# Optimization experiments

Measured on AMD Instinct MI355X. Metric: run time of the kernel, lower is better.

## Reference

```python
import jax, jax.numpy as jnp
import numpy as np

B, F, V, K, D, H = 16384, 26, 100000, 16, 13, 400
IN_DIM = F * K + D  # 429
EPS = 1e-5


def _bn(x, g, b):
    # BatchNorm1d in training mode: batch statistics (biased var, like torch)
    m = jnp.mean(x, axis=0)
    v = jnp.mean((x - m) ** 2, axis=0)
    return g * (x - m) / jnp.sqrt(v + EPS) + b


def setup_inputs() -> dict:
    key = jax.random.key(0)
    ks = jax.random.split(key, 12)
    X_cat = jax.random.randint(ks[0], (B, F), 0, V)
    X_dense = jax.random.normal(ks[1], (B, D), dtype=jnp.float32)
    fm1_tables = jax.random.normal(ks[2], (F, V, 1), dtype=jnp.float32) * 0.01
    emb_tables = jax.random.normal(ks[3], (F, V, K), dtype=jnp.float32) * 0.01
    Wd = jax.random.normal(ks[4], (D, 1), dtype=jnp.float32) * 0.1
    bd = jnp.zeros((1,), jnp.float32)
    W1 = jax.random.normal(ks[5], (IN_DIM, H), dtype=jnp.float32) * (1.0 / np.sqrt(IN_DIM))
    b1 = jnp.zeros((H,), jnp.float32)
    g1 = jnp.ones((H,), jnp.float32)
    be1 = jnp.zeros((H,), jnp.float32)
    W2 = jax.random.normal(ks[6], (H, H), dtype=jnp.float32) * (1.0 / np.sqrt(H))
    b2 = jnp.zeros((H,), jnp.float32)
    g2 = jnp.ones((H,), jnp.float32)
    be2 = jnp.zeros((H,), jnp.float32)
    W3 = jax.random.normal(ks[7], (H, 1), dtype=jnp.float32) * (1.0 / np.sqrt(H))
    b3 = jnp.zeros((1,), jnp.float32)
    return dict(X_cat=X_cat, X_dense=X_dense, fm1_tables=fm1_tables,
                emb_tables=emb_tables, Wd=Wd, bd=bd, W1=W1, b1=b1, g1=g1,
                be1=be1, W2=W2, b2=b2, g2=g2, be2=be2, W3=W3, b3=b3)


def reference(X_cat, X_dense, fm1_tables, emb_tables, Wd, bd,
              W1, b1, g1, be1, W2, b2, g2, be2, W3, b3):
    gather = jax.vmap(lambda tab, idx: tab[idx], in_axes=(0, 1), out_axes=1)
    # 1st order: [B, F, 1] -> sum over fields -> [B, 1]
    y_1st = jnp.sum(gather(fm1_tables, X_cat), axis=1) + X_dense @ Wd + bd
    # 2nd order embeddings: [B, F, K]
    emb = gather(emb_tables, X_cat)
    s = jnp.sum(emb, axis=1)                 # [B, K]
    ix = s ** 2 - jnp.sum(emb ** 2, axis=1)  # [B, K]
    fm_y = 0.5 * jnp.sum(ix, axis=1, keepdims=True)
    # DNN on [flattened embeddings, dense]
    x = jnp.concatenate([emb.reshape(emb.shape[0], -1), X_dense], axis=1)
    h = jax.nn.relu(_bn(x @ W1 + b1, g1, be1))
    h = jax.nn.relu(_bn(h @ W2 + b2, g2, be2))
    dnn_y = h @ W3 + b3
    return y_1st + fm_y + dnn_y
```

## Files before the change

kernel.cpp:

```cpp
#include <hip/hip_runtime.h>
#include <stdint.h>

#define B_ROWS 16384
#define NF 26
#define NV 100000
#define ND 13
#define NH 400
#define XPAD 448
#define ZPAD 416
#define EPS 1e-5f

typedef __attribute__((ext_vector_type(8))) short short8;
typedef __attribute__((ext_vector_type(4))) float f32x4;
typedef __attribute__((ext_vector_type(4))) unsigned int uint4v;

__device__ inline float bf2f(unsigned short u) {
    union { unsigned int i; float f; } v; v.i = (unsigned int)u << 16; return v.f;
}
__device__ inline unsigned short f2bf(float f) {
    union { float f; unsigned int i; } v; v.f = f;
    return (unsigned short)((v.i + 0x7fff + ((v.i >> 16) & 1)) >> 16);
}

typedef __attribute__((address_space(1))) const unsigned int g_u32;
typedef __attribute__((address_space(3))) unsigned int l_u32;
__device__ __forceinline__ void gload_lds16(const void* g, void* l) {
    __builtin_amdgcn_global_load_lds((g_u32*)g, (l_u32*)l, 16, 0, 0);
}

#define X_OFF    0
#define Z1_OFF   14680064
#define W1S_OFF  28311552
#define W2S_OFF  28712960
#define BASE_OFF 29085696
#define ST_OFF   29151232

__global__ __launch_bounds__(256) void gather_prep(
    const int* __restrict__ Xcat, const float* __restrict__ Xdense,
    const float* __restrict__ fm1, const float* __restrict__ emb,
    const float* __restrict__ Wd, const float* __restrict__ bd,
    const float* __restrict__ W1, const float* __restrict__ W2,
    unsigned short* __restrict__ X, float* __restrict__ base,
    unsigned short* __restrict__ W1s, unsigned short* __restrict__ W2s,
    float* __restrict__ st)
{
    int tid = threadIdx.x;
    if (blockIdx.x >= 1024) {
        int c = (blockIdx.x - 1024) * 256 + tid;
        if (c < 256) {
            for (int i = tid; i < 6656; i += 256) st[i] = 0.f;
        }
        const float* W; unsigned short* dst; int K; int cc;
        if (c < 25088) { W = W1; dst = W1s; K = 429; cc = c; }
        else           { W = W2; dst = W2s; K = 400; cc = c - 25088; }
        int n  = cc % 448;
        int q  = (cc / 448) & 3;
        int kt = cc / 1792;
        unsigned short o[8];
        #pragma unroll
        for (int j = 0; j < 8; ++j) {
            int k = kt * 32 + q * 8 + j;
            float v = (n < NH && k < K) ? W[(size_t)k * NH + n] : 0.f;
            o[j] = f2bf(v);
        }
        *(uint4v*)(dst + (size_t)cc * 8) = *(uint4v*)o;
        return;
    }
    int r = blockIdx.x * 16 + (tid >> 4);
    int k = tid & 15;
    const int* idxp = Xcat + (size_t)r * NF;
    unsigned short* xrow = X + (size_t)r * XPAD;

    float s = 0.f, ss = 0.f;
    #pragma unroll
    for (int f = 0; f < NF; ++f) {
        int idx = idxp[f];
        float v = emb[((size_t)f * NV + idx) * 16 + k];
        s += v; ss += v * v;
        xrow[f * 16 + k] = f2bf(v);
    }
    float fmsum = fm1[(size_t)k * NV + idxp[k]];
    if (k < NF - 16) fmsum += fm1[(size_t)(k + 16) * NV + idxp[k + 16]];
    float dsum = 0.f;
    if (k < ND) {
        float xd = Xdense[(size_t)r * ND + k];
        dsum = xd * Wd[k];
        xrow[NF * 16 + k] = f2bf(xd);
    }
    xrow[429 + k] = 0;
    if (k < 3) xrow[445 + k] = 0;

    float ix = s * s - ss;
    float rf = fmsum, rd = dsum;
    #pragma unroll
    for (int off = 8; off; off >>= 1) {
        ix += __shfl_xor(ix, off, 16);
        rf += __shfl_xor(rf, off, 16);
        rd += __shfl_xor(rd, off, 16);
    }
    if (k == 0) base[r] = 0.5f * ix + rf + rd + bd[0];
}

template<int NT, int LDA, bool APPLY_BN>
__global__ __launch_bounds__(512, 2) void gemm_v5(
    const unsigned short* __restrict__ A,
    const unsigned short* __restrict__ Wst,
    const float* __restrict__ bias,
    const float* __restrict__ st_all,
    const float* __restrict__ g, const float* __restrict__ be,
    unsigned short* __restrict__ Z, int ldz, int padZ,
    float* __restrict__ st_out, int sumOff, int sqOff)
{
    __shared__ __align__(16) unsigned short slices[51200];
    __shared__ float alpha_s[416], beta_s[416];

    const int tid = threadIdx.x, bid = blockIdx.x;
    const int lane = tid & 63, wv = tid >> 6;
    const int rg = wv >> 2, w4 = wv & 3;
    const int l15 = lane & 15, qh = lane >> 4;
    const int cb = (w4 == 0) ? 0 : (112 + (w4 - 1) * 96);
    const int NFW = (w4 == 0) ? 7 : 6;
    const int soff = rg * 12800 + ((w4 == 0) ? 0 : (3584 + (w4 - 1) * 3072));
    const int arowA = bid * 64 + rg * 32 + l15;
    const int arowB = arowA + 16;

    if constexpr (APPLY_BN) {
        if (tid < 416) {
            int c = tid;
            float a = 0.f, b = 0.f;
            if (c < NH) {
                float gs = 0.f, gq = 0.f;
                #pragma unroll
                for (int cp = 0; cp < 4; ++cp) {
                    gs += st_all[cp * 1664 + c];
                    gq += st_all[cp * 1664 + 416 + c];
                }
                float mean = gs * (1.f / 16384.f);
                float var  = gq * (1.f / 16384.f) - mean * mean;
                a = g[c] * rsqrtf(var + EPS);
                b = be[c] - mean * a;
            }
            alpha_s[c] = a; beta_s[c] = b;
        }
        __syncthreads();
    }

    f32x4 acc0[7], acc1[7];
    #pragma unroll
    for (int i = 0; i < 7; ++i) { acc0[i] = f32x4{0,0,0,0}; acc1[i] = f32x4{0,0,0,0}; }

    auto stageW = [&](int kt, int buf) {
        unsigned short* sl = slices + buf * 25600 + soff;
        #pragma unroll
        for (int i = 0; i < 7; ++i) if (i < NFW) {
            int ci = (kt * 4 + qh) * 448 + cb + i * 16 + l15;
            gload_lds16(Wst + (size_t)ci * 8, sl + i * 512);
        }
    };
    auto ldA = [&](int kt, short8& a, short8& b) {
        a = *(const short8*)(A + (size_t)arowA * LDA + kt * 32 + qh * 8);
        b = *(const short8*)(A + (size_t)arowB * LDA + kt * 32 + qh * 8);
    };
    auto waitN = [&]() {
        if (w4 == 0) asm volatile("s_waitcnt vmcnt(9)" ::: "memory");
        else         asm volatile("s_waitcnt vmcnt(8)" ::: "memory");
        __builtin_amdgcn_sched_barrier(0);
    };
    auto wait0 = [&]() {
        asm volatile("s_waitcnt vmcnt(0)" ::: "memory");
        __builtin_amdgcn_sched_barrier(0);
    };
    auto waitlg = [&]() {
        asm volatile("s_waitcnt lgkmcnt(0)" ::: "memory");
        __builtin_amdgcn_sched_barrier(0);
    };

    auto phase = [&](int kt, int buf, bool last, bool issue,
                     short8& afA, short8& afB) {
        if (last) wait0(); else waitN();
        const unsigned short* sl = slices + buf * 25600 + soff;
        short8 bf[7];
        #pragma unroll
        for (int i = 0; i < 7; ++i) if (i < NFW)
            bf[i] = *(const short8*)(sl + i * 512 + lane * 8);
        short8 aA = afA, aB = afB;
        waitlg();
        if (issue) { stageW(kt + 2, buf); ldA(kt + 2, afA, afB); }
        if constexpr (APPLY_BN) {
            const int k0 = kt * 32 + qh * 8;
            #pragma unroll
            for (int j = 0; j < 8; ++j) {
                float al = alpha_s[k0 + j], bt = beta_s[k0 + j];
                aA[j] = (short)f2bf(fmaxf(0.f, al * bf2f((unsigned short)aA[j]) + bt));
                aB[j] = (short)f2bf(fmaxf(0.f, al * bf2f((unsigned short)aB[j]) + bt));
            }
        }
        #pragma unroll
        for (int i = 0; i < 7; ++i) if (i < NFW) {
            acc0[i] = __builtin_amdgcn_mfma_f32_16x16x32_bf16(aA, bf[i], acc0[i], 0, 0, 0);
            acc1[i] = __builtin_amdgcn_mfma_f32_16x16x32_bf16(aB, bf[i], acc1[i], 0, 0, 0);
        }
    };

    short8 afA0, afB0, afA1, afB1;
    stageW(0, 0); ldA(0, afA0, afB0);
    stageW(1, 1); ldA(1, afA1, afB1);

    int kt2 = 0;
    for (; kt2 + 3 < NT; kt2 += 2) {
        phase(kt2,     0, false, true, afA0, afB0);
        phase(kt2 + 1, 1, false, true, afA1, afB1);
    }
    if constexpr (NT % 2 == 0) {
        phase(NT - 2, 0, false, false, afA0, afB0);
        phase(NT - 1, 1, true,  false, afA1, afB1);
    } else {
        phase(NT - 3, 0, false, true,  afA0, afB0);
        phase(NT - 2, 1, false, false, afA1, afB1);
        phase(NT - 1, 0, true,  false, afA0, afB0);
    }

    float* stc = st_out + (bid & 3) * 1664;
    #pragma unroll
    for (int i = 0; i < 7; ++i) if (i < NFW) {
        int col = cb + i * 16 + l15;
        float bv = bias[col];
        float ps = 0.f, pq = 0.f;
        #pragma unroll
        for (int q = 0; q < 4; ++q) {
            float v0 = acc0[i][q] + bv;
            float v1 = acc1[i][q] + bv;
            Z[(size_t)(bid * 64 + rg * 32 + qh * 4 + q) * ldz + col] = f2bf(v0);
            Z[(size_t)(bid * 64 + rg * 32 + 16 + qh * 4 + q) * ldz + col] = f2bf(v1);
            ps += v0 + v1; pq += v0 * v0 + v1 * v1;
        }
        ps += __shfl_xor(ps, 16, 64); ps += __shfl_xor(ps, 32, 64);
        pq += __shfl_xor(pq, 16, 64); pq += __shfl_xor(pq, 32, 64);
        if (qh == 0) {
            atomicAdd(&stc[sumOff + col], ps);
            atomicAdd(&stc[sqOff + col], pq);
        }
    }
    if (padZ && w4 == 3) {
        #pragma unroll
        for (int rr = 0; rr < 8; ++rr)
            Z[(size_t)(bid * 64 + rg * 32 + rr * 4 + qh) * ldz + 400 + l15] = 0;
    }
}

__global__ __launch_bounds__(256) void final_kernel(
    const unsigned short* __restrict__ Z2,
    const float* __restrict__ st_all,
    const float* __restrict__ g2, const float* __restrict__ be2,
    const float* __restrict__ W3, const float* __restrict__ b3,
    const float* __restrict__ base, float* __restrict__ out)
{
    __shared__ float a2s[NH], b2s[NH], w3s[NH];
    int tid = threadIdx.x;
    for (int c = tid; c < NH; c += 256) {
        float gs = 0.f, gq = 0.f;
        #pragma unroll
        for (int cp = 0; cp < 4; ++cp) {
            gs += st_all[cp * 1664 + 832 + c];
            gq += st_all[cp * 1664 + 1248 + c];
        }
        float mean = gs * (1.f / 16384.f);
        float var  = gq * (1.f / 16384.f) - mean * mean;
        float a = g2[c] * rsqrtf(var + EPS);
        a2s[c] = a;
        b2s[c] = be2[c] - mean * a;
        w3s[c] = W3[c];
    }
    __syncthreads();
    int lane = tid & 63;
    int wv = tid >> 6;
    bool act = lane < 50;
    int cb = lane * 8;
    float al[8], bb[8], w3[8];
    #pragma unroll
    for (int j = 0; j < 8; ++j) {
        al[j] = act ? a2s[cb + j] : 0.f;
        bb[j] = act ? b2s[cb + j] : 0.f;
        w3[j] = act ? w3s[cb + j] : 0.f;
    }
    int r0 = blockIdx.x * 32 + wv * 8;
    float bias3 = b3[0];
    for (int t = 0; t < 8; t += 2) {
        int r = r0 + t;
        float acc0 = 0.f, acc1 = 0.f;
        if (act) {
            short8 z0 = *(const short8*)(Z2 + (size_t)r * ZPAD + cb);
            short8 z1 = *(const short8*)(Z2 + (size_t)(r + 1) * ZPAD + cb);
            #pragma unroll
            for (int j = 0; j < 8; ++j) {
                acc0 += fmaxf(0.f, al[j] * bf2f((unsigned short)z0[j]) + bb[j]) * w3[j];
                acc1 += fmaxf(0.f, al[j] * bf2f((unsigned short)z1[j]) + bb[j]) * w3[j];
            }
        }
        #pragma unroll
        for (int off = 32; off; off >>= 1) {
            acc0 += __shfl_xor(acc0, off, 64);
            acc1 += __shfl_xor(acc1, off, 64);
        }
        if (lane == 0) out[r] = base[r] + acc0 + bias3;
        if (lane == 1) out[r + 1] = base[r + 1] + acc1 + bias3;
    }
}

extern "C" void kernel_launch(void* const* d_in, const int* in_sizes, int n_in,
                              void* d_out, int out_size, void* d_ws, size_t ws_size,
                              hipStream_t stream)
{
    const int*   Xcat = (const int*)d_in[0];
    const float* Xd   = (const float*)d_in[1];
    const float* fm1  = (const float*)d_in[2];
    const float* emb  = (const float*)d_in[3];
    const float* Wd   = (const float*)d_in[4];
    const float* bd   = (const float*)d_in[5];
    const float* W1   = (const float*)d_in[6];
    const float* b1   = (const float*)d_in[7];
    const float* g1   = (const float*)d_in[8];
    const float* be1  = (const float*)d_in[9];
    const float* W2   = (const float*)d_in[10];
    const float* b2   = (const float*)d_in[11];
    const float* g2   = (const float*)d_in[12];
    const float* be2  = (const float*)d_in[13];
    const float* W3   = (const float*)d_in[14];
    const float* b3   = (const float*)d_in[15];

    char* ws = (char*)d_ws;
    unsigned short* X   = (unsigned short*)(ws + X_OFF);
    unsigned short* Z1  = (unsigned short*)(ws + Z1_OFF);
    unsigned short* Z2  = X;
    unsigned short* W1s = (unsigned short*)(ws + W1S_OFF);
    unsigned short* W2s = (unsigned short*)(ws + W2S_OFF);
    float* base = (float*)(ws + BASE_OFF);
    float* st   = (float*)(ws + ST_OFF);
    float* out  = (float*)d_out;

    gather_prep<<<1213, 256, 0, stream>>>(Xcat, Xd, fm1, emb, Wd, bd, W1, W2,
                                          X, base, W1s, W2s, st);

    gemm_v5<14, XPAD, false><<<256, 512, 0, stream>>>(
        X, W1s, b1, nullptr, nullptr, nullptr, Z1, ZPAD, 1, st, 0, 416);

    gemm_v5<13, ZPAD, true><<<256, 512, 0, stream>>>(
        Z1, W2s, b2, st, g1, be1, Z2, ZPAD, 0, st, 832, 1248);

    final_kernel<<<512, 256, 0, stream>>>(Z2, st, g2, be2, W3, b3, base, out);
}
```

Measured before the change: 72.64 us.

## Gather embeddings field-major per block and defer FM reductions to final kernel

The embedding gather is reorganised so each block handles one field over a chunk of rows, using bid&7 to pick fields and keep each table's accesses localised, instead of one block walking all 26 fields per row. Dense features are written by separate blocks with vectorised stores. The FM second-order term, first-order sums and dense dot product move into the final kernel, which rereads the bf16 X rows and a new per-field fm1 value buffer. Z2 gets its own workspace buffer so X survives until then. Numerics change slightly because the FM terms are now computed from bf16-rounded embeddings and dense values.

```diff
diff --git a/kernel.cpp b/kernel.cpp
--- a/kernel.cpp
+++ b/kernel.cpp
@@ -30,26 +30,42 @@
 
 #define X_OFF    0
 #define Z1_OFF   14680064
-#define W1S_OFF  28311552
-#define W2S_OFF  28712960
-#define BASE_OFF 29085696
-#define ST_OFF   29151232
+#define Z2_OFF   28311552
+#define W1S_OFF  41943040
+#define W2S_OFF  42344448
+#define FM1V_OFF 42717184
+#define ST_OFF   44421120
 
 __global__ __launch_bounds__(256) void gather_prep(
     const int* __restrict__ Xcat, const float* __restrict__ Xdense,
     const float* __restrict__ fm1, const float* __restrict__ emb,
-    const float* __restrict__ Wd, const float* __restrict__ bd,
     const float* __restrict__ W1, const float* __restrict__ W2,
-    unsigned short* __restrict__ X, float* __restrict__ base,
+    unsigned short* __restrict__ X, float* __restrict__ fm1v,
     unsigned short* __restrict__ W1s, unsigned short* __restrict__ W2s,
     float* __restrict__ st)
 {
-    int tid = threadIdx.x;
-    if (blockIdx.x >= 1024) {
-        int c = (blockIdx.x - 1024) * 256 + tid;
-        if (c < 256) {
+    const int tid = threadIdx.x;
+    const int bid = blockIdx.x;
+    if (bid >= 1853) {
+        int r = (bid - 1853) * 256 + tid;
+        unsigned short o[32];
+        #pragma unroll
+        for (int j = 0; j < 32; ++j) {
+            float v = (j < ND) ? Xdense[(size_t)r * ND + j] : 0.f;
+            o[j] = f2bf(v);
+        }
+        uint4v* dst = (uint4v*)(X + (size_t)r * XPAD + 416);
+        dst[0] = *(uint4v*)&o[0];
+        dst[1] = *(uint4v*)&o[8];
+        dst[2] = *(uint4v*)&o[16];
+        dst[3] = *(uint4v*)&o[24];
+        return;
+    }
+    if (bid >= 1664) {
+        if (bid == 1664) {
             for (int i = tid; i < 6656; i += 256) st[i] = 0.f;
         }
+        int c = (bid - 1664) * 256 + tid;
         const float* W; unsigned short* dst; int K; int cc;
         if (c < 25088) { W = W1; dst = W1s; K = 429; cc = c; }
         else           { W = W2; dst = W2s; K = 400; cc = c - 25088; }
@@ -66,39 +82,37 @@
         *(uint4v*)(dst + (size_t)cc * 8) = *(uint4v*)o;
         return;
     }
-    int r = blockIdx.x * 16 + (tid >> 4);
-    int k = tid & 15;
-    const int* idxp = Xcat + (size_t)r * NF;
-    unsigned short* xrow = X + (size_t)r * XPAD;
-
-    float s = 0.f, ss = 0.f;
-    #pragma unroll
-    for (int f = 0; f < NF; ++f) {
-        int idx = idxp[f];
-        float v = emb[((size_t)f * NV + idx) * 16 + k];
-        s += v; ss += v * v;
-        xrow[f * 16 + k] = f2bf(v);
-    }
-    float fmsum = fm1[(size_t)k * NV + idxp[k]];
-    if (k < NF - 16) fmsum += fm1[(size_t)(k + 16) * NV + idxp[k + 16]];
-    float dsum = 0.f;
-    if (k < ND) {
-        float xd = Xdense[(size_t)r * ND + k];
-        dsum = xd * Wd[k];
-        xrow[NF * 16 + k] = f2bf(xd);
-    }
-    xrow[429 + k] = 0;
-    if (k < 3) xrow[445 + k] = 0;
-
-    float ix = s * s - ss;
-    float rf = fmsum, rd = dsum;
-    #pragma unroll
-    for (int off = 8; off; off >>= 1) {
-        ix += __shfl_xor(ix, off, 16);
-        rf += __shfl_xor(rf, off, 16);
-        rd += __shfl_xor(rd, off, 16);
-    }
-    if (k == 0) base[r] = 0.5f * ix + rf + rd + bd[0];
+    const int x = bid & 7;
+    const int s = bid >> 3;
+    const int nf = (x < 2) ? 4 : 3;
+    const int nc = 208 / nf;
+    const int fi = s / nc;
+    if (fi >= nf) return;
+    const int f = x + 8 * fi;
+    const int chunk = s - fi * nc;
+    const int rpc = (B_ROWS + nc - 1) / nc;
+    const int r0 = chunk * rpc;
+    const int r1 = (r0 + rpc < B_ROWS) ? r0 + rpc : B_ROWS;
+
+    const int k = tid & 15, rr = tid >> 4;
+    const float* et = emb + (size_t)f * NV * 16;
+    const float* ft = fm1 + (size_t)f * NV;
+    float* fv = fm1v + (size_t)f * B_ROWS;
+
+    for (int r = r0 + rr; r < r1; r += 32) {
+        int rb = r + 16;
+        bool okb = rb < r1;
+        int idx0 = Xcat[(size_t)r * NF + f];
+        int idx1 = okb ? Xcat[(size_t)rb * NF + f] : idx0;
+        float v0 = et[(size_t)idx0 * 16 + k];
+        float v1 = et[(size_t)idx1 * 16 + k];
+        X[(size_t)r * XPAD + f * 16 + k] = f2bf(v0);
+        if (okb) X[(size_t)rb * XPAD + f * 16 + k] = f2bf(v1);
+        if (k == 0) {
+            fv[r] = ft[idx0];
+            if (okb) fv[rb] = ft[idx1];
+        }
+    }
 }
 
 template<int NT, int LDA, bool APPLY_BN>
@@ -253,9 +267,13 @@
     const float* __restrict__ st_all,
     const float* __restrict__ g2, const float* __restrict__ be2,
     const float* __restrict__ W3, const float* __restrict__ b3,
-    const float* __restrict__ base, float* __restrict__ out)
+    const unsigned short* __restrict__ X, const float* __restrict__ fm1v,
+    const float* __restrict__ Wd, const float* __restrict__ bd,
+    float* __restrict__ out)
 {
     __shared__ float a2s[NH], b2s[NH], w3s[NH];
+    __shared__ float extra_s[32];
+    __shared__ float wd_s[16];
     int tid = threadIdx.x;
     for (int c = tid; c < NH; c += 256) {
         float gs = 0.f, gq = 0.f;
@@ -271,17 +289,72 @@
         b2s[c] = be2[c] - mean * a;
         w3s[c] = W3[c];
     }
+    if (tid < 16) wd_s[tid] = (tid < ND) ? Wd[tid] : 0.f;
     __syncthreads();
+
+    {
+        int rloc = tid >> 3, oct = tid & 7;
+        size_t rgl = (size_t)blockIdx.x * 32 + rloc;
+        const unsigned short* xr = X + rgl * XPAD;
+        float s16[16];
+        #pragma unroll
+        for (int i = 0; i < 16; ++i) s16[i] = 0.f;
+        float ssq = 0.f, fmsum = 0.f, dsum = 0.f;
+        #pragma unroll
+        for (int ff = 0; ff < 4; ++ff) {
+            int f = oct + ff * 8;
+            if (f < NF) {
+                short8 a = *(const short8*)(xr + f * 16);
+                short8 b = *(const short8*)(xr + f * 16 + 8);
+                #pragma unroll
+                for (int j = 0; j < 8; ++j) {
+                    float va = bf2f((unsigned short)a[j]);
+                    float vb = bf2f((unsigned short)b[j]);
+                    s16[j] += va; s16[8 + j] += vb;
+                    ssq += va * va + vb * vb;
+                }
+                fmsum += fm1v[(size_t)f * B_ROWS + rgl];
+            }
+        }
+        if (oct == 0) {
+            short8 d0 = *(const short8*)(xr + 416);
+            short8 d1 = *(const short8*)(xr + 424);
+            #pragma unroll
+            for (int j = 0; j < 8; ++j) dsum += bf2f((unsigned short)d0[j]) * wd_s[j];
+            #pragma unroll
+            for (int j = 0; j < 5; ++j) dsum += bf2f((unsigned short)d1[j]) * wd_s[8 + j];
+        }
+        #pragma unroll
+        for (int i = 0; i < 16; ++i) {
+            s16[i] += __shfl_xor(s16[i], 1, 64);
+            s16[i] += __shfl_xor(s16[i], 2, 64);
+            s16[i] += __shfl_xor(s16[i], 4, 64);
+        }
+        ssq += __shfl_xor(ssq, 1, 64);
+        ssq += __shfl_xor(ssq, 2, 64);
+        ssq += __shfl_xor(ssq, 4, 64);
+        fmsum += __shfl_xor(fmsum, 1, 64);
+        fmsum += __shfl_xor(fmsum, 2, 64);
+        fmsum += __shfl_xor(fmsum, 4, 64);
+        if (oct == 0) {
+            float sq = 0.f;
+            #pragma unroll
+            for (int i = 0; i < 16; ++i) sq += s16[i] * s16[i];
+            extra_s[rloc] = 0.5f * (sq - ssq) + fmsum + dsum + bd[0];
+        }
+    }
+    __syncthreads();
+
     int lane = tid & 63;
     int wv = tid >> 6;
     bool act = lane < 50;
-    int cb = lane * 8;
+    int cbx = lane * 8;
     float al[8], bb[8], w3[8];
     #pragma unroll
     for (int j = 0; j < 8; ++j) {
-        al[j] = act ? a2s[cb + j] : 0.f;
-        bb[j] = act ? b2s[cb + j] : 0.f;
-        w3[j] = act ? w3s[cb + j] : 0.f;
+        al[j] = act ? a2s[cbx + j] : 0.f;
+        bb[j] = act ? b2s[cbx + j] : 0.f;
+        w3[j] = act ? w3s[cbx + j] : 0.f;
     }
     int r0 = blockIdx.x * 32 + wv * 8;
     float bias3 = b3[0];
@@ -289,8 +362,8 @@
         int r = r0 + t;
         float acc0 = 0.f, acc1 = 0.f;
         if (act) {
-            short8 z0 = *(const short8*)(Z2 + (size_t)r * ZPAD + cb);
-            short8 z1 = *(const short8*)(Z2 + (size_t)(r + 1) * ZPAD + cb);
+            short8 z0 = *(const short8*)(Z2 + (size_t)r * ZPAD + cbx);
+            short8 z1 = *(const short8*)(Z2 + (size_t)(r + 1) * ZPAD + cbx);
             #pragma unroll
             for (int j = 0; j < 8; ++j) {
                 acc0 += fmaxf(0.f, al[j] * bf2f((unsigned short)z0[j]) + bb[j]) * w3[j];
@@ -302,8 +375,8 @@
             acc0 += __shfl_xor(acc0, off, 64);
             acc1 += __shfl_xor(acc1, off, 64);
         }
-        if (lane == 0) out[r] = base[r] + acc0 + bias3;
-        if (lane == 1) out[r + 1] = base[r + 1] + acc1 + bias3;
+        if (lane == 0) out[r] = extra_s[wv * 8 + t] + acc0 + bias3;
+        if (lane == 1) out[r + 1] = extra_s[wv * 8 + t + 1] + acc1 + bias3;
     }
 }
 
@@ -329,17 +402,17 @@
     const float* b3   = (const float*)d_in[15];
 
     char* ws = (char*)d_ws;
-    unsigned short* X   = (unsigned short*)(ws + X_OFF);
-    unsigned short* Z1  = (unsigned short*)(ws + Z1_OFF);
-    unsigned short* Z2  = X;
-    unsigned short* W1s = (unsigned short*)(ws + W1S_OFF);
-    unsigned short* W2s = (unsigned short*)(ws + W2S_OFF);
-    float* base = (float*)(ws + BASE_OFF);
+    unsigned short* X    = (unsigned short*)(ws + X_OFF);
+    unsigned short* Z1   = (unsigned short*)(ws + Z1_OFF);
+    unsigned short* Z2   = (unsigned short*)(ws + Z2_OFF);
+    unsigned short* W1s  = (unsigned short*)(ws + W1S_OFF);
+    unsigned short* W2s  = (unsigned short*)(ws + W2S_OFF);
+    float* fm1v = (float*)(ws + FM1V_OFF);
     float* st   = (float*)(ws + ST_OFF);
     float* out  = (float*)d_out;
 
-    gather_prep<<<1213, 256, 0, stream>>>(Xcat, Xd, fm1, emb, Wd, bd, W1, W2,
-                                          X, base, W1s, W2s, st);
+    gather_prep<<<1917, 256, 0, stream>>>(Xcat, Xd, fm1, emb, W1, W2,
+                                          X, fm1v, W1s, W2s, st);
 
     gemm_v5<14, XPAD, false><<<256, 512, 0, stream>>>(
         X, W1s, b1, nullptr, nullptr, nullptr, Z1, ZPAD, 1, st, 0, 416);
@@ -347,5 +420,6 @@
     gemm_v5<13, ZPAD, true><<<256, 512, 0, stream>>>(
         Z1, W2s, b2, st, g1, be1, Z2, ZPAD, 0, st, 832, 1248);
 
-    final_kernel<<<512, 256, 0, stream>>>(Z2, st, g2, be2, W3, b3, base, out);
-}
+    final_kernel<<<512, 256, 0, stream>>>(Z2, st, g2, be2, W3, b3,
+                                          X, fm1v, Wd, bd, out);
+}
```

Result: slower. 78.18 us (+7.6%).

## Fuse second GEMM with final BN2/ReLU/W3 via cooperative grid sync

Applied to the files above, without the earlier changes.

Replaces the second GEMM kernel plus the separate final kernel with one cooperative kernel. It computes the layer-2 GEMM, accumulates the BN2 statistics, does a grid-wide sync, then applies BN2, ReLU and the W3 dot product directly from the accumulators in registers. This removes the write and re-read of the Z2 activation and one kernel launch. In exchange it adds a grid barrier, needs all 256 blocks to be co-resident for the cooperative launch, and holds the accumulators in registers across the sync.

```diff
diff --git a/kernel.cpp b/kernel.cpp
--- a/kernel.cpp
+++ b/kernel.cpp
@@ -1,5 +1,8 @@
 #include <hip/hip_runtime.h>
+#include <hip/hip_cooperative_groups.h>
 #include <stdint.h>
+
+namespace cg = cooperative_groups;
 
 #define B_ROWS 16384
 #define NF 26
@@ -248,62 +251,191 @@
     }
 }
 
-__global__ __launch_bounds__(256) void final_kernel(
-    const unsigned short* __restrict__ Z2,
-    const float* __restrict__ st_all,
+__global__ __launch_bounds__(512, 2) void gemm2_final(
+    const unsigned short* __restrict__ A,
+    const unsigned short* __restrict__ Wst,
+    const float* __restrict__ b2,
+    float* __restrict__ st,
+    const float* __restrict__ g1, const float* __restrict__ be1,
     const float* __restrict__ g2, const float* __restrict__ be2,
     const float* __restrict__ W3, const float* __restrict__ b3,
     const float* __restrict__ base, float* __restrict__ out)
 {
-    __shared__ float a2s[NH], b2s[NH], w3s[NH];
-    int tid = threadIdx.x;
-    for (int c = tid; c < NH; c += 256) {
+    cg::grid_group grid = cg::this_grid();
+    __shared__ __align__(16) unsigned short slices[51200];
+    __shared__ float alpha_s[416], beta_s[416];
+    __shared__ float rowacc[64 * 4];
+
+    const int tid = threadIdx.x, bid = blockIdx.x;
+    const int lane = tid & 63, wv = tid >> 6;
+    const int rg = wv >> 2, w4 = wv & 3;
+    const int l15 = lane & 15, qh = lane >> 4;
+    const int cb = (w4 == 0) ? 0 : (112 + (w4 - 1) * 96);
+    const int NFW = (w4 == 0) ? 7 : 6;
+    const int soff = rg * 12800 + ((w4 == 0) ? 0 : (3584 + (w4 - 1) * 3072));
+    const int arowA = bid * 64 + rg * 32 + l15;
+    const int arowB = arowA + 16;
+
+    if (tid < 416) {
+        int c = tid;
+        float a = 0.f, b = 0.f;
+        if (c < NH) {
+            float gs = 0.f, gq = 0.f;
+            #pragma unroll
+            for (int cp = 0; cp < 4; ++cp) {
+                gs += st[cp * 1664 + c];
+                gq += st[cp * 1664 + 416 + c];
+            }
+            float mean = gs * (1.f / 16384.f);
+            float var  = gq * (1.f / 16384.f) - mean * mean;
+            a = g1[c] * rsqrtf(var + EPS);
+            b = be1[c] - mean * a;
+        }
+        alpha_s[c] = a; beta_s[c] = b;
+    }
+    __syncthreads();
+
+    f32x4 acc0[7], acc1[7];
+    #pragma unroll
+    for (int i = 0; i < 7; ++i) { acc0[i] = f32x4{0,0,0,0}; acc1[i] = f32x4{0,0,0,0}; }
+
+    auto stageW = [&](int kt, int buf) {
+        unsigned short* sl = slices + buf * 25600 + soff;
+        #pragma unroll
+        for (int i = 0; i < 7; ++i) if (i < NFW) {
+            int ci = (kt * 4 + qh) * 448 + cb + i * 16 + l15;
+            gload_lds16(Wst + (size_t)ci * 8, sl + i * 512);
+        }
+    };
+    auto ldA = [&](int kt, short8& a, short8& b) {
+        a = *(const short8*)(A + (size_t)arowA * ZPAD + kt * 32 + qh * 8);
+        b = *(const short8*)(A + (size_t)arowB * ZPAD + kt * 32 + qh * 8);
+    };
+    auto waitN = [&]() {
+        if (w4 == 0) asm volatile("s_waitcnt vmcnt(9)" ::: "memory");
+        else         asm volatile("s_waitcnt vmcnt(8)" ::: "memory");
+        __builtin_amdgcn_sched_barrier(0);
+    };
+    auto wait0 = [&]() {
+        asm volatile("s_waitcnt vmcnt(0)" ::: "memory");
+        __builtin_amdgcn_sched_barrier(0);
+    };
+    auto waitlg = [&]() {
+        asm volatile("s_waitcnt lgkmcnt(0)" ::: "memory");
+        __builtin_amdgcn_sched_barrier(0);
+    };
+
+    auto phase = [&](int kt, int buf, bool last, bool issue,
+                     short8& afA, short8& afB) {
+        if (last) wait0(); else waitN();
+        const unsigned short* sl = slices + buf * 25600 + soff;
+        short8 bf[7];
+        #pragma unroll
+        for (int i = 0; i < 7; ++i) if (i < NFW)
+            bf[i] = *(const short8*)(sl + i * 512 + lane * 8);
+        short8 aA = afA, aB = afB;
+        waitlg();
+        if (issue) { stageW(kt + 2, buf); ldA(kt + 2, afA, afB); }
+        {
+            const int k0 = kt * 32 + qh * 8;
+            #pragma unroll
+            for (int j = 0; j < 8; ++j) {
+                float al = alpha_s[k0 + j], bt = beta_s[k0 + j];
+                aA[j] = (short)f2bf(fmaxf(0.f, al * bf2f((unsigned short)aA[j]) + bt));
+                aB[j] = (short)f2bf(fmaxf(0.f, al * bf2f((unsigned short)aB[j]) + bt));
+            }
+        }
+        #pragma unroll
+        for (int i = 0; i < 7; ++i) if (i < NFW) {
+            acc0[i] = __builtin_amdgcn_mfma_f32_16x16x32_bf16(aA, bf[i], acc0[i], 0, 0, 0);
+            acc1[i] = __builtin_amdgcn_mfma_f32_16x16x32_bf16(aB, bf[i], acc1[i], 0, 0, 0);
+        }
+    };
+
+    short8 afA0, afB0, afA1, afB1;
+    stageW(0, 0); ldA(0, afA0, afB0);
+    stageW(1, 1); ldA(1, afA1, afB1);
+
+    int kt2 = 0;
+    for (; kt2 + 3 < 13; kt2 += 2) {
+        phase(kt2,     0, false, true, afA0, afB0);
+        phase(kt2 + 1, 1, false, true, afA1, afB1);
+    }
+    phase(10, 0, false, true,  afA0, afB0);
+    phase(11, 1, false, false, afA1, afB1);
+    phase(12, 0, true,  false, afA0, afB0);
+
+    float* stc = st + (bid & 3) * 1664;
+    #pragma unroll
+    for (int i = 0; i < 7; ++i) if (i < NFW) {
+        int col = cb + i * 16 + l15;
+        float bv = b2[col];
+        float ps = 0.f, pq = 0.f;
+        #pragma unroll
+        for (int q = 0; q < 4; ++q) {
+            float v0 = acc0[i][q] + bv;
+            float v1 = acc1[i][q] + bv;
+            ps += v0 + v1; pq += v0 * v0 + v1 * v1;
+        }
+        ps += __shfl_xor(ps, 16, 64); ps += __shfl_xor(ps, 32, 64);
+        pq += __shfl_xor(pq, 16, 64); pq += __shfl_xor(pq, 32, 64);
+        if (qh == 0) {
+            atomicAdd(&stc[832 + col], ps);
+            atomicAdd(&stc[1248 + col], pq);
+        }
+    }
+    grid.sync();
+
+    if (tid < NH) {
+        int c = tid;
         float gs = 0.f, gq = 0.f;
         #pragma unroll
         for (int cp = 0; cp < 4; ++cp) {
-            gs += st_all[cp * 1664 + 832 + c];
-            gq += st_all[cp * 1664 + 1248 + c];
+            gs += st[cp * 1664 + 832 + c];
+            gq += st[cp * 1664 + 1248 + c];
         }
         float mean = gs * (1.f / 16384.f);
         float var  = gq * (1.f / 16384.f) - mean * mean;
         float a = g2[c] * rsqrtf(var + EPS);
-        a2s[c] = a;
-        b2s[c] = be2[c] - mean * a;
-        w3s[c] = W3[c];
+        alpha_s[c] = a;
+        beta_s[c]  = be2[c] - mean * a;
     }
     __syncthreads();
-    int lane = tid & 63;
-    int wv = tid >> 6;
-    bool act = lane < 50;
-    int cb = lane * 8;
-    float al[8], bb[8], w3[8];
-    #pragma unroll
-    for (int j = 0; j < 8; ++j) {
-        al[j] = act ? a2s[cb + j] : 0.f;
-        bb[j] = act ? b2s[cb + j] : 0.f;
-        w3[j] = act ? w3s[cb + j] : 0.f;
-    }
-    int r0 = blockIdx.x * 32 + wv * 8;
-    float bias3 = b3[0];
-    for (int t = 0; t < 8; t += 2) {
-        int r = r0 + t;
-        float acc0 = 0.f, acc1 = 0.f;
-        if (act) {
-            short8 z0 = *(const short8*)(Z2 + (size_t)r * ZPAD + cb);
-            short8 z1 = *(const short8*)(Z2 + (size_t)(r + 1) * ZPAD + cb);
+
+    {
+        float bv[7], w3v[7], av[7], btv[7];
+        #pragma unroll
+        for (int i = 0; i < 7; ++i) if (i < NFW) {
+            int col = cb + i * 16 + l15;
+            bv[i] = b2[col]; w3v[i] = W3[col];
+            av[i] = alpha_s[col]; btv[i] = beta_s[col];
+        }
+        #pragma unroll
+        for (int q = 0; q < 4; ++q) {
+            float p0 = 0.f, p1 = 0.f;
             #pragma unroll
-            for (int j = 0; j < 8; ++j) {
-                acc0 += fmaxf(0.f, al[j] * bf2f((unsigned short)z0[j]) + bb[j]) * w3[j];
-                acc1 += fmaxf(0.f, al[j] * bf2f((unsigned short)z1[j]) + bb[j]) * w3[j];
-            }
-        }
-        #pragma unroll
-        for (int off = 32; off; off >>= 1) {
-            acc0 += __shfl_xor(acc0, off, 64);
-            acc1 += __shfl_xor(acc1, off, 64);
-        }
-        if (lane == 0) out[r] = base[r] + acc0 + bias3;
-        if (lane == 1) out[r + 1] = base[r + 1] + acc1 + bias3;
+            for (int i = 0; i < 7; ++i) if (i < NFW) {
+                float v0 = acc0[i][q] + bv[i];
+                float v1 = acc1[i][q] + bv[i];
+                p0 += fmaxf(0.f, av[i] * v0 + btv[i]) * w3v[i];
+                p1 += fmaxf(0.f, av[i] * v1 + btv[i]) * w3v[i];
+            }
+            p0 += __shfl_xor(p0, 1, 64); p0 += __shfl_xor(p0, 2, 64);
+            p0 += __shfl_xor(p0, 4, 64); p0 += __shfl_xor(p0, 8, 64);
+            p1 += __shfl_xor(p1, 1, 64); p1 += __shfl_xor(p1, 2, 64);
+            p1 += __shfl_xor(p1, 4, 64); p1 += __shfl_xor(p1, 8, 64);
+            if (l15 == 0) {
+                rowacc[(rg * 32 + qh * 4 + q) * 4 + w4] = p0;
+                rowacc[(rg * 32 + 16 + qh * 4 + q) * 4 + w4] = p1;
+            }
+        }
+    }
+    __syncthreads();
+    if (tid < 64) {
+        int r = bid * 64 + tid;
+        float s = rowacc[tid * 4] + rowacc[tid * 4 + 1]
+                + rowacc[tid * 4 + 2] + rowacc[tid * 4 + 3];
+        out[r] = base[r] + s + b3[0];
     }
 }
 
@@ -331,7 +463,6 @@
     char* ws = (char*)d_ws;
     unsigned short* X   = (unsigned short*)(ws + X_OFF);
     unsigned short* Z1  = (unsigned short*)(ws + Z1_OFF);
-    unsigned short* Z2  = X;
     unsigned short* W1s = (unsigned short*)(ws + W1S_OFF);
     unsigned short* W2s = (unsigned short*)(ws + W2S_OFF);
     float* base = (float*)(ws + BASE_OFF);
@@ -344,8 +475,11 @@
     gemm_v5<14, XPAD, false><<<256, 512, 0, stream>>>(
         X, W1s, b1, nullptr, nullptr, nullptr, Z1, ZPAD, 1, st, 0, 416);
 
-    gemm_v5<13, ZPAD, true><<<256, 512, 0, stream>>>(
-        Z1, W2s, b2, st, g1, be1, Z2, ZPAD, 0, st, 832, 1248);
-
-    final_kernel<<<512, 256, 0, stream>>>(Z2, st, g2, be2, W3, b3, base, out);
-}
+    void* args[] = {
+        (void*)&Z1, (void*)&W2s, (void*)&b2, (void*)&st,
+        (void*)&g1, (void*)&be1, (void*)&g2, (void*)&be2,
+        (void*)&W3, (void*)&b3, (void*)&base, (void*)&out
+    };
+    hipLaunchCooperativeKernel((const void*)gemm2_final, dim3(256), dim3(512),
+                               args, 0, stream);
+}
```

Result: slower. 102.6 us (+41.3%).
